# Kernel optimization log

Measured on AMD Instinct MI355X. Metric: run time of the kernel, lower is better.

The kernel has to match this reference:

```python
import jax, jax.numpy as jnp
import numpy as np

H = 12          # num_heads
LENS_T = 64     # template tokens
LENS_S = 256    # search tokens
KEEP = int(0.7 * LENS_S)  # 179 kept search tokens


def _ln(x, s, b):
    mu = jnp.mean(x, axis=-1, keepdims=True)
    var = jnp.mean(jnp.square(x - mu), axis=-1, keepdims=True)
    return (x - mu) / jnp.sqrt(var + 1e-5) * s + b


def setup_inputs() -> dict:
    key = jax.random.key(0)
    ks = jax.random.split(key, 8)
    B, C, Hh = 32, 768, 3072
    N = LENS_T + LENS_S
    w = lambda k, shape: jax.random.normal(k, shape, jnp.float32) * 0.02
    return {
        "x": jax.random.normal(ks[0], (B, N, C), jnp.float32),
        "global_index_t": jnp.tile(jnp.arange(LENS_T, dtype=jnp.int32), (B, 1)),
        "global_index_s": jnp.tile(jnp.arange(LENS_S, dtype=jnp.int32), (B, 1)),
        "norm1_s": jnp.ones((C,), jnp.float32), "norm1_b": jnp.zeros((C,), jnp.float32),
        "qkv_w": w(ks[1], (C, 3 * C)), "qkv_b": jnp.zeros((3 * C,), jnp.float32),
        "proj_w": w(ks[2], (C, C)), "proj_b": jnp.zeros((C,), jnp.float32),
        "norm2_s": jnp.ones((C,), jnp.float32), "norm2_b": jnp.zeros((C,), jnp.float32),
        "fc1_w": w(ks[3], (C, Hh)), "fc1_b": jnp.zeros((Hh,), jnp.float32),
        "fc2_w": w(ks[4], (Hh, C)), "fc2_b": jnp.zeros((C,), jnp.float32),
        "gcn_w": w(ks[5], (C, C)), "gcn_b": jnp.zeros((C,), jnp.float32),
        "norm3_s": jnp.ones((C,), jnp.float32), "norm3_b": jnp.zeros((C,), jnp.float32),
    }


def reference(x, global_index_t, global_index_s,
              norm1_s, norm1_b, qkv_w, qkv_b, proj_w, proj_b,
              norm2_s, norm2_b, fc1_w, fc1_b, fc2_w, fc2_b,
              gcn_w, gcn_b, norm3_s, norm3_b):
    B, N, C = x.shape
    hd = C // H
    scale = hd ** -0.5

    # --- attention (attn weights explicitly materialized) ---
    h = _ln(x, norm1_s, norm1_b)
    qkv = (h @ qkv_w + qkv_b).reshape(B, N, 3, H, hd).transpose(2, 0, 3, 1, 4)
    q, k, v = qkv[0], qkv[1], qkv[2]                      # [B,H,N,hd]
    attn = jax.nn.softmax(jnp.einsum('bhqd,bhkd->bhqk', q, k) * scale, axis=-1)
    xa = jnp.einsum('bhqk,bhkd->bhqd', attn, v).transpose(0, 2, 1, 3).reshape(B, N, C)
    xa = xa @ proj_w + proj_b
    x = x + xa

    # --- MLP ---
    x_res = x
    h2 = _ln(x, norm2_s, norm2_b)
    h2 = jax.nn.gelu(h2 @ fc1_w + fc1_b, approximate=False) @ fc2_w + fc2_b
    x = x_res + h2

    # --- GCN using template<->search attention as adjacency ---
    # adjacency = [[0, w_ts], [w_ts^T, 0]]; exploit block sparsity instead of
    # materializing the dense [B,N,N] matrix.
    w_ts = jnp.sum(attn[:, :, :LENS_T, LENS_T:], axis=1) / H   # [B,T,S]
    w_ts = jax.nn.softmax(w_ts, axis=2)
    support = x @ gcn_w + gcn_b
    out_t = jnp.einsum('bts,bsd->btd', w_ts, support[:, LENS_T:])   # top block
    out_s = jnp.einsum('bts,btd->bsd', w_ts, support[:, :LENS_T])   # bottom block
    x = jnp.concatenate([out_t, out_s], axis=1)
    x = x + _ln(x, norm3_s, norm3_b)

    # --- top-k token pruning on search tokens ---
    score_s = jnp.mean(attn[:, :, :LENS_T, LENS_T:], axis=(1, 2))   # [B,S]
    order = jnp.argsort(-score_s, axis=1)
    keep_indices = order[:, :KEEP]
    removed_index_s = order[:, KEEP:]
    gs_new = jnp.take_along_axis(global_index_s, keep_indices, axis=1)
    idx = jnp.concatenate([global_index_t.astype(jnp.int32), keep_indices + LENS_T], axis=1)
    x = jnp.take_along_axis(x, jnp.broadcast_to(idx[..., None], (B, idx.shape[1], C)), axis=1)
    return (x, global_index_t, gs_new, removed_index_s, attn)
```

## Files before the change

### kernel.cpp

```cpp
#include <hip/hip_runtime.h>
#include <math.h>

#define NKEEP 179
#define NREM  77
#define NOUT_ROWS 243

typedef __bf16 bf16x8 __attribute__((ext_vector_type(8)));
typedef float f32x4 __attribute__((ext_vector_type(4)));

__device__ __forceinline__ unsigned short f2bf(float f) {
  unsigned u = __builtin_bit_cast(unsigned, f);
  u = (u + 0x7FFFu + ((u >> 16) & 1u)) >> 16;
  return (unsigned short)u;
}

__device__ __forceinline__ void gload_lds16(const void* g, void* l) {
  __builtin_amdgcn_global_load_lds((const __attribute__((address_space(1))) void*)g,
                                   (__attribute__((address_space(3))) void*)l,
                                   16, 0, 0);
}

template<int RESID, int OUTMODE>
__global__ __launch_bounds__(256)
void ln_kernel(const float* __restrict__ in, const float* __restrict__ gs,
               const float* __restrict__ gb, void* __restrict__ outp,
               void* __restrict__ outp2) {
  int row = blockIdx.x;
  const float* p = in + (size_t)row * 768;
  int tid = threadIdx.x;
  float v0 = p[tid], v1 = p[tid + 256], v2 = p[tid + 512];
  __shared__ double rs[256], rq[256];
  double d0 = v0, d1 = v1, d2 = v2;
  rs[tid] = d0 + d1 + d2;
  rq[tid] = d0 * d0 + d1 * d1 + d2 * d2;
  __syncthreads();
  for (int st = 128; st > 0; st >>= 1) {
    if (tid < st) { rs[tid] += rs[tid + st]; rq[tid] += rq[tid + st]; }
    __syncthreads();
  }
  double mu  = rs[0] * (1.0 / 768.0);
  double var = rq[0] * (1.0 / 768.0) - mu * mu;
  float rstd = (float)rsqrt(var + 1e-5);
  float muf = (float)mu;
  float y0 = (v0 - muf) * rstd * gs[tid]       + gb[tid];
  float y1 = (v1 - muf) * rstd * gs[tid + 256] + gb[tid + 256];
  float y2 = (v2 - muf) * rstd * gs[tid + 512] + gb[tid + 512];
  if (RESID) { y0 += v0; y1 += v1; y2 += v2; }
  if (OUTMODE == 0 || OUTMODE == 2) {
    float* o = (float*)outp + (size_t)row * 768;
    o[tid] = y0; o[tid + 256] = y1; o[tid + 512] = y2;
  }
  if (OUTMODE == 1) {
    unsigned short* o = (unsigned short*)outp + (size_t)row * 768;
    o[tid] = f2bf(y0); o[tid + 256] = f2bf(y1); o[tid + 512] = f2bf(y2);
  }
  if (OUTMODE == 2) {
    unsigned short* o = (unsigned short*)outp2 + (size_t)row * 768;
    o[tid] = f2bf(y0); o[tid + 256] = f2bf(y1); o[tid + 512] = f2bf(y2);
  }
}

__global__ __launch_bounds__(256)
void wtrans_kernel(const float* __restrict__ W, unsigned short* __restrict__ Wt,
                   int K, int N) {
  __shared__ float t[32][33];
  int n0 = blockIdx.x * 32, k0 = blockIdx.y * 32;
  int tid = threadIdx.x;
#pragma unroll
  for (int p = 0; p < 4; p++) {
    int idx = tid + p * 256;
    int r = idx >> 5, c = idx & 31;
    t[r][c] = W[(size_t)(k0 + r) * N + n0 + c];
  }
  __syncthreads();
#pragma unroll
  for (int p = 0; p < 4; p++) {
    int idx = tid + p * 256;
    int r = idx >> 5, c = idx & 31;
    Wt[(size_t)(n0 + r) * K + k0 + c] = f2bf(t[c][r]);
  }
}

template<int ACT, int RES, int OUTBF>
__global__ __launch_bounds__(256)
void gemm_bf16_kernel(const unsigned short* __restrict__ A,
                      const unsigned short* __restrict__ Bt,
                      const float* __restrict__ bias, const float* __restrict__ res,
                      void* __restrict__ outp, int M, int K, int N) {
  __shared__ unsigned short Al[128 * 64];
  __shared__ unsigned short Bl[128 * 64];
  int tid = threadIdx.x;
  int lane = tid & 63, wid = tid >> 6;
  int wr = wid >> 1, wc = wid & 1;
  int bm0 = blockIdx.y * 128, bn0 = blockIdx.x * 128;

  int r8 = lane >> 3;
  int csw = lane & 7;
  int csrc = csw ^ r8;

  const unsigned short* Abase = A + (size_t)bm0 * K + (size_t)csrc * 8;
  const unsigned short* Bbase = Bt + (size_t)bn0 * K + (size_t)csrc * 8;

  f32x4 acc[4][4] = {};

  int mrow = lane & 15;
  int kch = lane >> 4;
  int key = mrow & 7;

  for (int k0 = 0; k0 < K; k0 += 64) {
#pragma unroll
    for (int i = 0; i < 4; i++) {
      int rr = wid * 32 + i * 8;
      gload_lds16(Abase + (size_t)(rr + r8) * K + k0, Al + rr * 64);
      gload_lds16(Bbase + (size_t)(rr + r8) * K + k0, Bl + rr * 64);
    }
    __syncthreads();
#pragma unroll
    for (int ks = 0; ks < 2; ks++) {
      bf16x8 af[4], bfr[4];
#pragma unroll
      for (int f = 0; f < 4; f++) {
        int ra = wr * 64 + f * 16 + mrow;
        int ca = (ks * 4 + kch) ^ key;
        af[f] = *reinterpret_cast<const bf16x8*>(&Al[ra * 64 + ca * 8]);
        int rb = wc * 64 + f * 16 + mrow;
        bfr[f] = *reinterpret_cast<const bf16x8*>(&Bl[rb * 64 + ca * 8]);
      }
#pragma unroll
      for (int fm = 0; fm < 4; fm++)
#pragma unroll
        for (int fn = 0; fn < 4; fn++)
          acc[fm][fn] = __builtin_amdgcn_mfma_f32_16x16x32_bf16(
              af[fm], bfr[fn], acc[fm][fn], 0, 0, 0);
    }
    __syncthreads();
  }
#pragma unroll
  for (int fm = 0; fm < 4; fm++) {
#pragma unroll
    for (int j = 0; j < 4; j++) {
      int row = bm0 + wr * 64 + fm * 16 + (lane >> 4) * 4 + j;
#pragma unroll
      for (int fn = 0; fn < 4; fn++) {
        int col = bn0 + wc * 64 + fn * 16 + (lane & 15);
        float c = acc[fm][fn][j] + bias[col];
        if (ACT == 1) c = 0.5f * c * (1.0f + erff(c * 0.70710678118654752f));
        if (RES) c += res[(size_t)row * N + col];
        if (OUTBF) ((unsigned short*)outp)[(size_t)row * N + col] = f2bf(c);
        else       ((float*)outp)[(size_t)row * N + col] = c;
      }
    }
  }
}

__global__ __launch_bounds__(256)
void gemm_qkv_bf16_kernel(const unsigned short* __restrict__ A,
                          const unsigned short* __restrict__ Bt,
                          const float* __restrict__ bias,
                          float* __restrict__ Qb, float* __restrict__ Kb,
                          float* __restrict__ Vb) {
  __shared__ unsigned short Al[128 * 64];
  __shared__ unsigned short Bl[128 * 64];
  const int K = 768;
  int tid = threadIdx.x;
  int lane = tid & 63, wid = tid >> 6;
  int wr = wid >> 1, wc = wid & 1;
  int bm0 = blockIdx.y * 128, bn0 = blockIdx.x * 128;

  int r8 = lane >> 3;
  int csw = lane & 7;
  int csrc = csw ^ r8;

  const unsigned short* Abase = A + (size_t)bm0 * K + (size_t)csrc * 8;
  const unsigned short* Bbase = Bt + (size_t)bn0 * K + (size_t)csrc * 8;

  f32x4 acc[4][4] = {};
  int mrow = lane & 15;
  int kch = lane >> 4;
  int key = mrow & 7;

  for (int k0 = 0; k0 < K; k0 += 64) {
#pragma unroll
    for (int i = 0; i < 4; i++) {
      int rr = wid * 32 + i * 8;
      gload_lds16(Abase + (size_t)(rr + r8) * K + k0, Al + rr * 64);
      gload_lds16(Bbase + (size_t)(rr + r8) * K + k0, Bl + rr * 64);
    }
    __syncthreads();
#pragma unroll
    for (int ks = 0; ks < 2; ks++) {
      bf16x8 af[4], bfr[4];
#pragma unroll
      for (int f = 0; f < 4; f++) {
        int ra = wr * 64 + f * 16 + mrow;
        int ca = (ks * 4 + kch) ^ key;
        af[f] = *reinterpret_cast<const bf16x8*>(&Al[ra * 64 + ca * 8]);
        int rb = wc * 64 + f * 16 + mrow;
        bfr[f] = *reinterpret_cast<const bf16x8*>(&Bl[rb * 64 + ca * 8]);
      }
#pragma unroll
      for (int fm = 0; fm < 4; fm++)
#pragma unroll
        for (int fn = 0; fn < 4; fn++)
          acc[fm][fn] = __builtin_amdgcn_mfma_f32_16x16x32_bf16(
              af[fm], bfr[fn], acc[fm][fn], 0, 0, 0);
    }
    __syncthreads();
  }
#pragma unroll
  for (int fm = 0; fm < 4; fm++) {
#pragma unroll
    for (int j = 0; j < 4; j++) {
      int row = bm0 + wr * 64 + fm * 16 + (lane >> 4) * 4 + j;
      int b = row / 320, nr = row - b * 320;
#pragma unroll
      for (int fn = 0; fn < 4; fn++) {
        int col = bn0 + wc * 64 + fn * 16 + (lane & 15);
        int sel = col / 768;
        int rem = col - sel * 768;
        int h = rem >> 6, d = rem & 63;
        float* dstb = (sel == 0) ? Qb : (sel == 1) ? Kb : Vb;
        dstb[(((size_t)(b * 12 + h) * 320 + nr) << 6) + d] = acc[fm][fn][j] + bias[col];
      }
    }
  }
}

template<int ROWMAP>
__global__ __launch_bounds__(256)
void gemm_prec_kernel(const float* __restrict__ A, const float* __restrict__ W,
                      const float* __restrict__ bias, int colOff,
                      float* __restrict__ Dst) {
  __shared__ float As[64][20];
  __shared__ float Bs[16][64];
  int tid = threadIdx.x;
  int tx = tid & 15, ty = tid >> 4;
  int bm0 = blockIdx.y * 64, bn0 = blockIdx.x * 64;
  int sm = tid >> 2, sc4 = tid & 3;
  int br = tid >> 4, bc4 = tid & 15;
  int arow;
  if (ROWMAP) { int m = bm0 + sm; arow = (m >> 6) * 320 + (m & 63); }
  else        { arow = bm0 + sm; }
  const float* Aptr = A + (size_t)arow * 768 + sc4 * 4;
  const float* Wptr = W + (size_t)br * 2304 + colOff + bn0 + bc4 * 4;

  double master[4][4] = {};
  for (int k0 = 0; k0 < 768; k0 += 16) {
    float4 av = *(const float4*)(Aptr + k0);
    float4 bv = *(const float4*)(Wptr + (size_t)k0 * 2304);
    __syncthreads();
    *(float4*)&As[sm][sc4 * 4] = av;
    *(float4*)&Bs[br][bc4 * 4] = bv;
    __syncthreads();
    float chunk[4][4] = {};
#pragma unroll
    for (int kk = 0; kk < 16; kk++) {
      float a[4], bb[4];
      *(float4*)bb = *(const float4*)&Bs[kk][tx * 4];
#pragma unroll
      for (int i = 0; i < 4; i++) a[i] = As[ty * 4 + i][kk];
#pragma unroll
      for (int i = 0; i < 4; i++)
#pragma unroll
        for (int j = 0; j < 4; j++) chunk[i][j] = fmaf(a[i], bb[j], chunk[i][j]);
    }
#pragma unroll
    for (int i = 0; i < 4; i++)
#pragma unroll
      for (int j = 0; j < 4; j++) master[i][j] += (double)chunk[i][j];
  }
  int n0 = bn0 + tx * 4;
  int h = n0 >> 6, d = n0 & 63;
#pragma unroll
  for (int i = 0; i < 4; i++) {
    int m = bm0 + ty * 4 + i;
    int b, nr;
    if (ROWMAP) { b = m >> 6; nr = m & 63; }
    else        { b = m / 320; nr = m - b * 320; }
    float* dst = Dst + (((size_t)(b * 12 + h) * 320 + nr) << 6) + d;
    float4 v;
    v.x = (float)master[i][0] + bias[colOff + n0];
    v.y = (float)master[i][1] + bias[colOff + n0 + 1];
    v.z = (float)master[i][2] + bias[colOff + n0 + 2];
    v.w = (float)master[i][3] + bias[colOff + n0 + 3];
    *(float4*)dst = v;
  }
}

__global__ __launch_bounds__(256)
void attn_fused_kernel(const float* __restrict__ Qb, const float* __restrict__ Kb,
                       const float* __restrict__ Vb, float* __restrict__ attn,
                       unsigned short* __restrict__ xa) {
  __shared__ float Qs[64][68];
  __shared__ float Ks[64][68];
  int qt = blockIdx.x, h = blockIdx.y, b = blockIdx.z;
  int bh = b * 12 + h;
  int q0 = qt * 64;
  int t = threadIdx.x;
  int tx = t & 15, ty = t >> 4;
  const float* Qg = Qb + (((size_t)bh * 320 + q0) << 6);
  const float* Kg = Kb + (((size_t)bh * 320) << 6);
  const float* Vg = Vb + (((size_t)bh * 320) << 6);
  float* attn_bh = attn + ((size_t)bh * 320 + q0) * 320;

  {
    int r = t >> 2, c = (t & 3) * 16;
    const float* src = Qg + (r << 6) + c;
#pragma unroll
    for (int i = 0; i < 4; i++)
      *(float4*)&Qs[r][c + i * 4] = *(const float4*)(src + i * 4);
  }

  float mrow[4] = {-1e30f, -1e30f, -1e30f, -1e30f};
  for (int kc = 0; kc < 5; ++kc) {
    __syncthreads();
    {
      int r = t >> 2, c = (t & 3) * 16;
      const float* src = Kg + ((size_t)(kc * 64 + r) << 6) + c;
#pragma unroll
      for (int i = 0; i < 4; i++)
        *(float4*)&Ks[r][c + i * 4] = *(const float4*)(src + i * 4);
    }
    __syncthreads();
    float acc[4][4] = {};
#pragma unroll 4
    for (int d0 = 0; d0 < 64; d0 += 4) {
      float4 qv[4], kv[4];
#pragma unroll
      for (int i = 0; i < 4; i++) qv[i] = *(const float4*)&Qs[ty * 4 + i][d0];
#pragma unroll
      for (int j = 0; j < 4; j++) kv[j] = *(const float4*)&Ks[tx * 4 + j][d0];
#pragma unroll
      for (int i = 0; i < 4; i++)
#pragma unroll
        for (int j = 0; j < 4; j++) {
          acc[i][j] = fmaf(qv[i].x, kv[j].x, acc[i][j]);
          acc[i][j] = fmaf(qv[i].y, kv[j].y, acc[i][j]);
          acc[i][j] = fmaf(qv[i].z, kv[j].z, acc[i][j]);
          acc[i][j] = fmaf(qv[i].w, kv[j].w, acc[i][j]);
        }
    }
#pragma unroll
    for (int i = 0; i < 4; i++) {
      float4 sv;
      sv.x = acc[i][0] * 0.125f; sv.y = acc[i][1] * 0.125f;
      sv.z = acc[i][2] * 0.125f; sv.w = acc[i][3] * 0.125f;
      mrow[i] = fmaxf(mrow[i], fmaxf(fmaxf(sv.x, sv.y), fmaxf(sv.z, sv.w)));
      *(float4*)&attn_bh[(size_t)(ty * 4 + i) * 320 + kc * 64 + tx * 4] = sv;
    }
  }
#pragma unroll
  for (int i = 0; i < 4; i++) {
    mrow[i] = fmaxf(mrow[i], __shfl_xor(mrow[i], 1, 16));
    mrow[i] = fmaxf(mrow[i], __shfl_xor(mrow[i], 2, 16));
    mrow[i] = fmaxf(mrow[i], __shfl_xor(mrow[i], 4, 16));
    mrow[i] = fmaxf(mrow[i], __shfl_xor(mrow[i], 8, 16));
  }
  __syncthreads();

  double lsum[4] = {0.0, 0.0, 0.0, 0.0};
#pragma unroll
  for (int i = 0; i < 4; i++) {
    float* rp = attn_bh + (size_t)(ty * 4 + i) * 320;
    for (int u = 0; u < 20; u++) {
      int k = tx + 16 * u;
      float e = expf(rp[k] - mrow[i]);
      rp[k] = e;
      lsum[i] += (double)e;
    }
  }
#pragma unroll
  for (int i = 0; i < 4; i++) {
    lsum[i] += __shfl_xor(lsum[i], 1, 16);
    lsum[i] += __shfl_xor(lsum[i], 2, 16);
    lsum[i] += __shfl_xor(lsum[i], 4, 16);
    lsum[i] += __shfl_xor(lsum[i], 8, 16);
  }
  float inv[4];
#pragma unroll
  for (int i = 0; i < 4; i++) inv[i] = (float)(1.0 / lsum[i]);
  __syncthreads();

#pragma unroll
  for (int i = 0; i < 4; i++) {
    float* rp = attn_bh + (size_t)(ty * 4 + i) * 320;
    for (int u = 0; u < 20; u++) {
      int k = tx + 16 * u;
      rp[k] *= inv[i];
    }
  }

  float acc2[4][4] = {};
  for (int kc = 0; kc < 5; ++kc) {
    __syncthreads();
    {
      int r = t >> 2, c = (t & 3) * 16;
      const float* src = Vg + ((size_t)(kc * 64 + r) << 6) + c;
#pragma unroll
      for (int i = 0; i < 4; i++)
        *(float4*)&Ks[r][c + i * 4] = *(const float4*)(src + i * 4);
    }
    __syncthreads();
#pragma unroll 4
    for (int kk4 = 0; kk4 < 16; ++kk4) {
      int k = kc * 64 + kk4 * 4;
      float4 pv[4], vv[4];
#pragma unroll
      for (int i = 0; i < 4; i++)
        pv[i] = *(const float4*)&attn_bh[(size_t)(ty * 4 + i) * 320 + k];
#pragma unroll
      for (int l = 0; l < 4; l++) vv[l] = *(const float4*)&Ks[kk4 * 4 + l][tx * 4];
#pragma unroll
      for (int i = 0; i < 4; i++) {
        acc2[i][0] = fmaf(pv[i].x, vv[0].x, acc2[i][0]);
        acc2[i][1] = fmaf(pv[i].x, vv[0].y, acc2[i][1]);
        acc2[i][2] = fmaf(pv[i].x, vv[0].z, acc2[i][2]);
        acc2[i][3] = fmaf(pv[i].x, vv[0].w, acc2[i][3]);
        acc2[i][0] = fmaf(pv[i].y, vv[1].x, acc2[i][0]);
        acc2[i][1] = fmaf(pv[i].y, vv[1].y, acc2[i][1]);
        acc2[i][2] = fmaf(pv[i].y, vv[1].z, acc2[i][2]);
        acc2[i][3] = fmaf(pv[i].y, vv[1].w, acc2[i][3]);
        acc2[i][0] = fmaf(pv[i].z, vv[2].x, acc2[i][0]);
        acc2[i][1] = fmaf(pv[i].z, vv[2].y, acc2[i][1]);
        acc2[i][2] = fmaf(pv[i].z, vv[2].z, acc2[i][2]);
        acc2[i][3] = fmaf(pv[i].z, vv[2].w, acc2[i][3]);
        acc2[i][0] = fmaf(pv[i].w, vv[3].x, acc2[i][0]);
        acc2[i][1] = fmaf(pv[i].w, vv[3].y, acc2[i][1]);
        acc2[i][2] = fmaf(pv[i].w, vv[3].z, acc2[i][2]);
        acc2[i][3] = fmaf(pv[i].w, vv[3].w, acc2[i][3]);
      }
    }
  }
#pragma unroll
  for (int i = 0; i < 4; i++) {
    unsigned short* dst = xa + (size_t)(b * 320 + q0 + ty * 4 + i) * 768 + h * 64 + tx * 4;
    uint2 pk;
    pk.x = (unsigned)f2bf(acc2[i][0]) | ((unsigned)f2bf(acc2[i][1]) << 16);
    pk.y = (unsigned)f2bf(acc2[i][2]) | ((unsigned)f2bf(acc2[i][3]) << 16);
    *(uint2*)dst = pk;
  }
}

__global__ __launch_bounds__(256)
void wts_kernel(const float* __restrict__ attn, float* __restrict__ wts) {
  int bid = blockIdx.x;
  int tt = bid & 63, b = bid >> 6;
  int s = threadIdx.x;
  float acc = 0.0f;
  const float* base = attn + (((size_t)(b * 12)) * 320 + tt) * 320 + 64 + s;
#pragma unroll
  for (int h = 0; h < 12; h++) acc += base[(size_t)h * 320 * 320];
  acc *= (1.0f / 12.0f);
  __shared__ float red[256];
  red[s] = acc; __syncthreads();
  for (int st = 128; st > 0; st >>= 1) {
    if (s < st) red[s] = fmaxf(red[s], red[s + st]);
    __syncthreads();
  }
  float m = red[0]; __syncthreads();
  float e = expf(acc - m);
  red[s] = e; __syncthreads();
  for (int st = 128; st > 0; st >>= 1) {
    if (s < st) red[s] += red[s + st];
    __syncthreads();
  }
  wts[(size_t)bid * 256 + s] = e / red[0];
}

__global__ __launch_bounds__(256)
void out_t_kernel(const float* __restrict__ wts, const float* __restrict__ sup,
                  float* __restrict__ x3) {
  int idx = blockIdx.x * 256 + threadIdx.x;
  int c = idx % 768;
  int tt = (idx / 768) % 64;
  int b = idx / (768 * 64);
  const float* wrow = wts + (size_t)(b * 64 + tt) * 256;
  const float* sp = sup + ((size_t)(b * 320 + 64)) * 768 + c;
  float acc = 0.0f;
  for (int s = 0; s < 256; s++) acc = fmaf(wrow[s], sp[(size_t)s * 768], acc);
  x3[((size_t)(b * 320 + tt)) * 768 + c] = acc;
}

__global__ __launch_bounds__(256)
void out_s_kernel(const float* __restrict__ wts, const float* __restrict__ sup,
                  float* __restrict__ x3) {
  int idx = blockIdx.x * 256 + threadIdx.x;
  int c = idx % 768;
  int s = (idx / 768) % 256;
  int b = idx / (768 * 256);
  const float* wp = wts + (size_t)(b * 64) * 256 + s;
  const float* sp = sup + ((size_t)(b * 320)) * 768 + c;
  float acc = 0.0f;
#pragma unroll 4
  for (int tt = 0; tt < 64; tt++) acc = fmaf(wp[(size_t)tt * 256], sp[(size_t)tt * 768], acc);
  x3[((size_t)(b * 320 + 64 + s)) * 768 + c] = acc;
}

__global__ __launch_bounds__(256)
void score_part_kernel(const float* __restrict__ attn, double* __restrict__ part) {
  int h = blockIdx.x, b = blockIdx.y;
  int s = threadIdx.x;
  const float* base = attn + (((size_t)(b * 12 + h)) * 320) * 320 + 64 + s;
  double acc = 0.0;
  for (int tt = 0; tt < 64; tt++) acc += (double)base[(size_t)tt * 320];
  part[((size_t)(b * 12 + h)) * 256 + s] = acc;
}

__global__ __launch_bounds__(256)
void score_final_kernel(const double* __restrict__ part, const int* __restrict__ git,
                        const int* __restrict__ gis, int* __restrict__ order_ws,
                        float* __restrict__ out_git, float* __restrict__ out_gs,
                        float* __restrict__ out_rm) {
  int b = blockIdx.x, s = threadIdx.x;
  double acc = 0.0;
#pragma unroll
  for (int h = 0; h < 12; h++) acc += part[((size_t)(b * 12 + h)) * 256 + s];
  __shared__ double sc[256];
  __shared__ int ord[256];
  sc[s] = acc;
  __syncthreads();
  double my = sc[s];
  int r = 0;
  for (int i = 0; i < 256; i++) {
    double si = sc[i];
    r += (si > my) || (si == my && i < s);
  }
  ord[r] = s;
  __syncthreads();
  int o = ord[s];
  order_ws[b * 256 + s] = o;
  if (s < NKEEP) out_gs[b * NKEEP + s] = (float)gis[b * 256 + o];
  else           out_rm[b * NREM + (s - NKEEP)] = (float)o;
  if (s < 64)    out_git[b * 64 + s] = (float)git[b * 64 + s];
}

__global__ __launch_bounds__(256)
void gather_kernel(const float* __restrict__ x3, const int* __restrict__ git,
                   const int* __restrict__ order_ws, float* __restrict__ out) {
  int bid = blockIdx.x;
  int j = bid % NOUT_ROWS, b = bid / NOUT_ROWS;
  int src = (j < 64) ? git[b * 64 + j] : (order_ws[b * 256 + (j - 64)] + 64);
  const float* p = x3 + ((size_t)(b * 320 + src)) * 768;
  float* o = out + ((size_t)(b * NOUT_ROWS + j)) * 768;
  int tid = threadIdx.x;
  o[tid] = p[tid]; o[tid + 256] = p[tid + 256]; o[tid + 512] = p[tid + 512];
}

extern "C" void kernel_launch(void* const* d_in, const int* in_sizes, int n_in,
                              void* d_out, int out_size, void* d_ws, size_t ws_size,
                              hipStream_t stream) {
  (void)in_sizes; (void)n_in; (void)out_size; (void)ws_size;
  const float* x      = (const float*)d_in[0];
  const int*   git    = (const int*)d_in[1];
  const int*   gis    = (const int*)d_in[2];
  const float* n1s    = (const float*)d_in[3];
  const float* n1b    = (const float*)d_in[4];
  const float* qkv_w  = (const float*)d_in[5];
  const float* qkv_b  = (const float*)d_in[6];
  const float* proj_w = (const float*)d_in[7];
  const float* proj_b = (const float*)d_in[8];
  const float* n2s    = (const float*)d_in[9];
  const float* n2b    = (const float*)d_in[10];
  const float* fc1_w  = (const float*)d_in[11];
  const float* fc1_b  = (const float*)d_in[12];
  const float* fc2_w  = (const float*)d_in[13];
  const float* fc2_b  = (const float*)d_in[14];
  const float* gcn_w  = (const float*)d_in[15];
  const float* gcn_b  = (const float*)d_in[16];
  const float* n3s    = (const float*)d_in[17];
  const float* n3b    = (const float*)d_in[18];

  float* out     = (float*)d_out;
  float* out_x   = out;
  float* out_git = out + 5971968;
  float* out_gs  = out + 5974016;
  float* out_rm  = out + 5979744;
  float* attn    = out + 5982208;

  float* w      = (float*)d_ws;
  float* bufA   = w;
  float* bufB   = w + 7864320;
  float* bufBIG = w + 15728640;
  float* Qbuf = bufBIG;
  float* Kbuf = bufBIG + 7864320;
  float* Vbuf = bufBIG + 15728640;
  unsigned short* ln1_bf = (unsigned short*)(bufBIG + 23592960);
  unsigned short* f1_bf = (unsigned short*)bufBIG;
  unsigned short* x2_bf = (unsigned short*)(bufBIG + 15728640);
  float* x3 = bufBIG + 19660800;
  unsigned short* wbf = (unsigned short*)(bufBIG + 27525120);
  unsigned short* proj_wt = wbf;
  unsigned short* fc1_wt  = wbf + 589824;
  unsigned short* fc2_wt  = fc1_wt + 2359296;
  unsigned short* gcn_wt  = fc2_wt + 2359296;
  unsigned short* qkv_wt  = gcn_wt + 589824;
  unsigned short* xa_bf = (unsigned short*)bufA;
  unsigned short* h2_bf = (unsigned short*)bufA;
  float* wts    = bufBIG + 31457280;
  int*   order_ws = (int*)(wts + 524288);
  double* partd  = (double*)(wts + 524288 + 8192);

  const int M = 10240;

  wtrans_kernel<<<dim3(24, 24), dim3(256), 0, stream>>>(proj_w, proj_wt, 768, 768);
  wtrans_kernel<<<dim3(96, 24), dim3(256), 0, stream>>>(fc1_w, fc1_wt, 768, 3072);
  wtrans_kernel<<<dim3(24, 96), dim3(256), 0, stream>>>(fc2_w, fc2_wt, 3072, 768);
  wtrans_kernel<<<dim3(24, 24), dim3(256), 0, stream>>>(gcn_w, gcn_wt, 768, 768);
  wtrans_kernel<<<dim3(72, 24), dim3(256), 0, stream>>>(qkv_w, qkv_wt, 768, 2304);

  ln_kernel<0, 2><<<dim3(M), dim3(256), 0, stream>>>(x, n1s, n1b, bufA, ln1_bf);
  gemm_qkv_bf16_kernel<<<dim3(18, 80), dim3(256), 0, stream>>>(
      ln1_bf, qkv_wt, qkv_b, Qbuf, Kbuf, Vbuf);
  gemm_prec_kernel<0><<<dim3(12, 160), dim3(256), 0, stream>>>(
      bufA, qkv_w, qkv_b, 768, Kbuf);
  gemm_prec_kernel<1><<<dim3(12, 32), dim3(256), 0, stream>>>(
      bufA, qkv_w, qkv_b, 0, Qbuf);
  attn_fused_kernel<<<dim3(5, 12, 32), dim3(256), 0, stream>>>(
      Qbuf, Kbuf, Vbuf, attn, xa_bf);
  gemm_bf16_kernel<0, 1, 0><<<dim3(768 / 128, M / 128), dim3(256), 0, stream>>>(
      xa_bf, proj_wt, proj_b, x, bufB, M, 768, 768);
  ln_kernel<0, 1><<<dim3(M), dim3(256), 0, stream>>>(bufB, n2s, n2b, h2_bf, nullptr);
  gemm_bf16_kernel<1, 0, 1><<<dim3(3072 / 128, M / 128), dim3(256), 0, stream>>>(
      h2_bf, fc1_wt, fc1_b, nullptr, f1_bf, M, 768, 3072);
  gemm_bf16_kernel<0, 1, 1><<<dim3(768 / 128, M / 128), dim3(256), 0, stream>>>(
      f1_bf, fc2_wt, fc2_b, bufB, x2_bf, M, 3072, 768);
  wts_kernel<<<dim3(32 * 64), dim3(256), 0, stream>>>(attn, wts);
  gemm_bf16_kernel<0, 0, 0><<<dim3(768 / 128, M / 128), dim3(256), 0, stream>>>(
      x2_bf, gcn_wt, gcn_b, nullptr, bufA, M, 768, 768);
  out_t_kernel<<<dim3(32 * 64 * 768 / 256), dim3(256), 0, stream>>>(wts, bufA, x3);
  out_s_kernel<<<dim3(32 * 256 * 768 / 256), dim3(256), 0, stream>>>(wts, bufA, x3);
  ln_kernel<1, 0><<<dim3(M), dim3(256), 0, stream>>>(x3, n3s, n3b, x3, nullptr);
  score_part_kernel<<<dim3(12, 32), dim3(256), 0, stream>>>(attn, partd);
  score_final_kernel<<<dim3(32), dim3(256), 0, stream>>>(partd, git, gis, order_ws,
                                                         out_git, out_gs, out_rm);
  gather_kernel<<<dim3(32 * NOUT_ROWS), dim3(256), 0, stream>>>(x3, git,
                                                                order_ws, out_x);
}
```

Baseline: 1.093 ms.

## Enlarge precise GEMM tile and keep attention scores in registers for softmax

The fp32/fp64-accumulating precise GEMM used for K and Q now computes 128x64 tiles with a 32-deep K step instead of 64x64 with 16. This doubles per-thread work, halves the grid and cuts barrier count. The attention kernel keeps the 4x20 score values per thread in registers through max, exp and normalisation and writes the attn matrix to global memory once. Previously it wrote, reread, rewrote, reread and rewrote it. The cost is higher register pressure from the larger double accumulator array and the score array, which may lower occupancy.

```diff
diff --git a/kernel.cpp b/kernel.cpp
--- a/kernel.cpp
+++ b/kernel.cpp
@@ -231,59 +231,91 @@
 void gemm_prec_kernel(const float* __restrict__ A, const float* __restrict__ W,
                       const float* __restrict__ bias, int colOff,
                       float* __restrict__ Dst) {
-  __shared__ float As[64][20];
-  __shared__ float Bs[16][64];
+  __shared__ float As[128][36];
+  __shared__ float Bs[32][68];
   int tid = threadIdx.x;
   int tx = tid & 15, ty = tid >> 4;
-  int bm0 = blockIdx.y * 64, bn0 = blockIdx.x * 64;
-  int sm = tid >> 2, sc4 = tid & 3;
-  int br = tid >> 4, bc4 = tid & 15;
-  int arow;
-  if (ROWMAP) { int m = bm0 + sm; arow = (m >> 6) * 320 + (m & 63); }
-  else        { arow = bm0 + sm; }
-  const float* Aptr = A + (size_t)arow * 768 + sc4 * 4;
-  const float* Wptr = W + (size_t)br * 2304 + colOff + bn0 + bc4 * 4;
-
-  double master[4][4] = {};
-  for (int k0 = 0; k0 < 768; k0 += 16) {
-    float4 av = *(const float4*)(Aptr + k0);
-    float4 bv = *(const float4*)(Wptr + (size_t)k0 * 2304);
-    __syncthreads();
-    *(float4*)&As[sm][sc4 * 4] = av;
-    *(float4*)&Bs[br][bc4 * 4] = bv;
-    __syncthreads();
-    float chunk[4][4] = {};
-#pragma unroll
-    for (int kk = 0; kk < 16; kk++) {
-      float a[4], bb[4];
-      *(float4*)bb = *(const float4*)&Bs[kk][tx * 4];
-#pragma unroll
-      for (int i = 0; i < 4; i++) a[i] = As[ty * 4 + i][kk];
-#pragma unroll
-      for (int i = 0; i < 4; i++)
-#pragma unroll
-        for (int j = 0; j < 4; j++) chunk[i][j] = fmaf(a[i], bb[j], chunk[i][j]);
-    }
-#pragma unroll
-    for (int i = 0; i < 4; i++)
-#pragma unroll
-      for (int j = 0; j < 4; j++) master[i][j] += (double)chunk[i][j];
+  int bm0 = blockIdx.y * 128, bn0 = blockIdx.x * 64;
+
+  int ar[4];
+#pragma unroll
+  for (int q = 0; q < 4; q++) {
+    int idx = tid + q * 256;
+    int r = idx >> 3;
+    int m = bm0 + r;
+    ar[q] = ROWMAP ? ((m >> 6) * 320 + (m & 63)) : m;
+  }
+  const float* Wbase = W + colOff + bn0;
+
+  double master[8][4] = {};
+  for (int k0 = 0; k0 < 768; k0 += 32) {
+    float4 av[4], bv[2];
+#pragma unroll
+    for (int q = 0; q < 4; q++) {
+      int idx = tid + q * 256;
+      av[q] = *(const float4*)(A + (size_t)ar[q] * 768 + k0 + (idx & 7) * 4);
+    }
+#pragma unroll
+    for (int q = 0; q < 2; q++) {
+      int idx = tid + q * 256;
+      int br = idx >> 4, bc4 = idx & 15;
+      bv[q] = *(const float4*)(Wbase + (size_t)(k0 + br) * 2304 + bc4 * 4);
+    }
+    __syncthreads();
+#pragma unroll
+    for (int q = 0; q < 4; q++) {
+      int idx = tid + q * 256;
+      *(float4*)&As[idx >> 3][(idx & 7) * 4] = av[q];
+    }
+#pragma unroll
+    for (int q = 0; q < 2; q++) {
+      int idx = tid + q * 256;
+      *(float4*)&Bs[idx >> 4][(idx & 15) * 4] = bv[q];
+    }
+    __syncthreads();
+#pragma unroll
+    for (int half = 0; half < 2; half++) {
+      float chunk[8][4] = {};
+#pragma unroll
+      for (int kk = 0; kk < 16; kk++) {
+        int kkk = half * 16 + kk;
+        float a[8], bb[4];
+        *(float4*)bb = *(const float4*)&Bs[kkk][tx * 4];
+#pragma unroll
+        for (int i = 0; i < 4; i++) {
+          a[i]     = As[ty * 4 + i][kkk];
+          a[4 + i] = As[64 + ty * 4 + i][kkk];
+        }
+#pragma unroll
+        for (int i = 0; i < 8; i++)
+#pragma unroll
+          for (int j = 0; j < 4; j++) chunk[i][j] = fmaf(a[i], bb[j], chunk[i][j]);
+      }
+#pragma unroll
+      for (int i = 0; i < 8; i++)
+#pragma unroll
+        for (int j = 0; j < 4; j++) master[i][j] += (double)chunk[i][j];
+    }
+    __syncthreads();
   }
   int n0 = bn0 + tx * 4;
   int h = n0 >> 6, d = n0 & 63;
 #pragma unroll
-  for (int i = 0; i < 4; i++) {
-    int m = bm0 + ty * 4 + i;
-    int b, nr;
-    if (ROWMAP) { b = m >> 6; nr = m & 63; }
-    else        { b = m / 320; nr = m - b * 320; }
-    float* dst = Dst + (((size_t)(b * 12 + h) * 320 + nr) << 6) + d;
-    float4 v;
-    v.x = (float)master[i][0] + bias[colOff + n0];
-    v.y = (float)master[i][1] + bias[colOff + n0 + 1];
-    v.z = (float)master[i][2] + bias[colOff + n0 + 2];
-    v.w = (float)master[i][3] + bias[colOff + n0 + 3];
-    *(float4*)dst = v;
+  for (int g = 0; g < 2; g++) {
+#pragma unroll
+    for (int i = 0; i < 4; i++) {
+      int m = bm0 + g * 64 + ty * 4 + i;
+      int b, nr;
+      if (ROWMAP) { b = m >> 6; nr = m & 63; }
+      else        { b = m / 320; nr = m - b * 320; }
+      float* dst = Dst + (((size_t)(b * 12 + h) * 320 + nr) << 6) + d;
+      float4 v;
+      v.x = (float)master[g * 4 + i][0] + bias[colOff + n0];
+      v.y = (float)master[g * 4 + i][1] + bias[colOff + n0 + 1];
+      v.z = (float)master[g * 4 + i][2] + bias[colOff + n0 + 2];
+      v.w = (float)master[g * 4 + i][3] + bias[colOff + n0 + 3];
+      *(float4*)dst = v;
+    }
   }
 }
 
@@ -311,7 +343,10 @@
       *(float4*)&Qs[r][c + i * 4] = *(const float4*)(src + i * 4);
   }
 
+  float s[4][20];
   float mrow[4] = {-1e30f, -1e30f, -1e30f, -1e30f};
+
+#pragma unroll
   for (int kc = 0; kc < 5; ++kc) {
     __syncthreads();
     {
@@ -342,11 +377,11 @@
     }
 #pragma unroll
     for (int i = 0; i < 4; i++) {
-      float4 sv;
-      sv.x = acc[i][0] * 0.125f; sv.y = acc[i][1] * 0.125f;
-      sv.z = acc[i][2] * 0.125f; sv.w = acc[i][3] * 0.125f;
-      mrow[i] = fmaxf(mrow[i], fmaxf(fmaxf(sv.x, sv.y), fmaxf(sv.z, sv.w)));
-      *(float4*)&attn_bh[(size_t)(ty * 4 + i) * 320 + kc * 64 + tx * 4] = sv;
+      float sx = acc[i][0] * 0.125f, sy = acc[i][1] * 0.125f;
+      float sz = acc[i][2] * 0.125f, sw = acc[i][3] * 0.125f;
+      mrow[i] = fmaxf(mrow[i], fmaxf(fmaxf(sx, sy), fmaxf(sz, sw)));
+      s[i][kc * 4 + 0] = sx; s[i][kc * 4 + 1] = sy;
+      s[i][kc * 4 + 2] = sz; s[i][kc * 4 + 3] = sw;
     }
   }
 #pragma unroll
@@ -356,19 +391,16 @@
     mrow[i] = fmaxf(mrow[i], __shfl_xor(mrow[i], 4, 16));
     mrow[i] = fmaxf(mrow[i], __shfl_xor(mrow[i], 8, 16));
   }
-  __syncthreads();
 
   double lsum[4] = {0.0, 0.0, 0.0, 0.0};
 #pragma unroll
-  for (int i = 0; i < 4; i++) {
-    float* rp = attn_bh + (size_t)(ty * 4 + i) * 320;
-    for (int u = 0; u < 20; u++) {
-      int k = tx + 16 * u;
-      float e = expf(rp[k] - mrow[i]);
-      rp[k] = e;
+  for (int i = 0; i < 4; i++)
+#pragma unroll
+    for (int c = 0; c < 20; c++) {
+      float e = expf(s[i][c] - mrow[i]);
+      s[i][c] = e;
       lsum[i] += (double)e;
     }
-  }
 #pragma unroll
   for (int i = 0; i < 4; i++) {
     lsum[i] += __shfl_xor(lsum[i], 1, 16);
@@ -379,16 +411,19 @@
   float inv[4];
 #pragma unroll
   for (int i = 0; i < 4; i++) inv[i] = (float)(1.0 / lsum[i]);
+
+#pragma unroll
+  for (int i = 0; i < 4; i++)
+#pragma unroll
+    for (int kc = 0; kc < 5; kc++) {
+      float4 sv;
+      sv.x = s[i][kc * 4 + 0] * inv[i];
+      sv.y = s[i][kc * 4 + 1] * inv[i];
+      sv.z = s[i][kc * 4 + 2] * inv[i];
+      sv.w = s[i][kc * 4 + 3] * inv[i];
+      *(float4*)&attn_bh[(size_t)(ty * 4 + i) * 320 + kc * 64 + tx * 4] = sv;
+    }
   __syncthreads();
-
-#pragma unroll
-  for (int i = 0; i < 4; i++) {
-    float* rp = attn_bh + (size_t)(ty * 4 + i) * 320;
-    for (int u = 0; u < 20; u++) {
-      int k = tx + 16 * u;
-      rp[k] *= inv[i];
-    }
-  }
 
   float acc2[4][4] = {};
   for (int kc = 0; kc < 5; ++kc) {
@@ -611,9 +646,9 @@
   ln_kernel<0, 2><<<dim3(M), dim3(256), 0, stream>>>(x, n1s, n1b, bufA, ln1_bf);
   gemm_qkv_bf16_kernel<<<dim3(18, 80), dim3(256), 0, stream>>>(
       ln1_bf, qkv_wt, qkv_b, Qbuf, Kbuf, Vbuf);
-  gemm_prec_kernel<0><<<dim3(12, 160), dim3(256), 0, stream>>>(
+  gemm_prec_kernel<0><<<dim3(12, 80), dim3(256), 0, stream>>>(
       bufA, qkv_w, qkv_b, 768, Kbuf);
-  gemm_prec_kernel<1><<<dim3(12, 32), dim3(256), 0, stream>>>(
+  gemm_prec_kernel<1><<<dim3(12, 16), dim3(256), 0, stream>>>(
       bufA, qkv_w, qkv_b, 0, Qbuf);
   attn_fused_kernel<<<dim3(5, 12, 32), dim3(256), 0, stream>>>(
       Qbuf, Kbuf, Vbuf, attn, xa_bf);
```

Result: slower. 1.304 ms (+19.3%).

## Skip redundant K columns in bf16 QKV GEMM and keep softmax scores in registers

Applied to the files above, without the earlier changes.

The bf16 QKV GEMM no longer computes the K third of the output, which was overwritten anyway by the higher-precision K GEMM. This cuts its grid from 18 to 12 column tiles. The attention kernel now holds the scaled scores for each thread in registers (4x20 floats) and writes the normalized attention to global memory once. Previously it did three read-modify-write passes over the attn buffer. This raises register pressure in the attention kernel, which may lower occupancy.

```diff
diff --git a/kernel.cpp b/kernel.cpp
--- a/kernel.cpp
+++ b/kernel.cpp
@@ -157,22 +157,23 @@
 void gemm_qkv_bf16_kernel(const unsigned short* __restrict__ A,
                           const unsigned short* __restrict__ Bt,
                           const float* __restrict__ bias,
-                          float* __restrict__ Qb, float* __restrict__ Kb,
-                          float* __restrict__ Vb) {
+                          float* __restrict__ Qb, float* __restrict__ Vb) {
   __shared__ unsigned short Al[128 * 64];
   __shared__ unsigned short Bl[128 * 64];
   const int K = 768;
   int tid = threadIdx.x;
   int lane = tid & 63, wid = tid >> 6;
   int wr = wid >> 1, wc = wid & 1;
-  int bm0 = blockIdx.y * 128, bn0 = blockIdx.x * 128;
+  int bx = blockIdx.x;
+  int colbase = (bx < 6) ? bx * 128 : (bx - 6) * 128 + 1536;
+  int bm0 = blockIdx.y * 128;
 
   int r8 = lane >> 3;
   int csw = lane & 7;
   int csrc = csw ^ r8;
 
   const unsigned short* Abase = A + (size_t)bm0 * K + (size_t)csrc * 8;
-  const unsigned short* Bbase = Bt + (size_t)bn0 * K + (size_t)csrc * 8;
+  const unsigned short* Bbase = Bt + (size_t)colbase * K + (size_t)csrc * 8;
 
   f32x4 acc[4][4] = {};
   int mrow = lane & 15;
@@ -215,11 +216,11 @@
       int b = row / 320, nr = row - b * 320;
 #pragma unroll
       for (int fn = 0; fn < 4; fn++) {
-        int col = bn0 + wc * 64 + fn * 16 + (lane & 15);
+        int col = colbase + wc * 64 + fn * 16 + (lane & 15);
         int sel = col / 768;
         int rem = col - sel * 768;
         int h = rem >> 6, d = rem & 63;
-        float* dstb = (sel == 0) ? Qb : (sel == 1) ? Kb : Vb;
+        float* dstb = (sel == 0) ? Qb : Vb;
         dstb[(((size_t)(b * 12 + h) * 320 + nr) << 6) + d] = acc[fm][fn][j] + bias[col];
       }
     }
@@ -311,7 +312,10 @@
       *(float4*)&Qs[r][c + i * 4] = *(const float4*)(src + i * 4);
   }
 
+  float s[4][20];
   float mrow[4] = {-1e30f, -1e30f, -1e30f, -1e30f};
+
+#pragma unroll
   for (int kc = 0; kc < 5; ++kc) {
     __syncthreads();
     {
@@ -342,11 +346,11 @@
     }
 #pragma unroll
     for (int i = 0; i < 4; i++) {
-      float4 sv;
-      sv.x = acc[i][0] * 0.125f; sv.y = acc[i][1] * 0.125f;
-      sv.z = acc[i][2] * 0.125f; sv.w = acc[i][3] * 0.125f;
-      mrow[i] = fmaxf(mrow[i], fmaxf(fmaxf(sv.x, sv.y), fmaxf(sv.z, sv.w)));
-      *(float4*)&attn_bh[(size_t)(ty * 4 + i) * 320 + kc * 64 + tx * 4] = sv;
+      float sx = acc[i][0] * 0.125f, sy = acc[i][1] * 0.125f;
+      float sz = acc[i][2] * 0.125f, sw = acc[i][3] * 0.125f;
+      mrow[i] = fmaxf(mrow[i], fmaxf(fmaxf(sx, sy), fmaxf(sz, sw)));
+      s[i][kc * 4 + 0] = sx; s[i][kc * 4 + 1] = sy;
+      s[i][kc * 4 + 2] = sz; s[i][kc * 4 + 3] = sw;
     }
   }
 #pragma unroll
@@ -356,19 +360,16 @@
     mrow[i] = fmaxf(mrow[i], __shfl_xor(mrow[i], 4, 16));
     mrow[i] = fmaxf(mrow[i], __shfl_xor(mrow[i], 8, 16));
   }
-  __syncthreads();
 
   double lsum[4] = {0.0, 0.0, 0.0, 0.0};
 #pragma unroll
-  for (int i = 0; i < 4; i++) {
-    float* rp = attn_bh + (size_t)(ty * 4 + i) * 320;
-    for (int u = 0; u < 20; u++) {
-      int k = tx + 16 * u;
-      float e = expf(rp[k] - mrow[i]);
-      rp[k] = e;
+  for (int i = 0; i < 4; i++)
+#pragma unroll
+    for (int c = 0; c < 20; c++) {
+      float e = expf(s[i][c] - mrow[i]);
+      s[i][c] = e;
       lsum[i] += (double)e;
     }
-  }
 #pragma unroll
   for (int i = 0; i < 4; i++) {
     lsum[i] += __shfl_xor(lsum[i], 1, 16);
@@ -379,16 +380,19 @@
   float inv[4];
 #pragma unroll
   for (int i = 0; i < 4; i++) inv[i] = (float)(1.0 / lsum[i]);
+
+#pragma unroll
+  for (int i = 0; i < 4; i++)
+#pragma unroll
+    for (int kc = 0; kc < 5; kc++) {
+      float4 sv;
+      sv.x = s[i][kc * 4 + 0] * inv[i];
+      sv.y = s[i][kc * 4 + 1] * inv[i];
+      sv.z = s[i][kc * 4 + 2] * inv[i];
+      sv.w = s[i][kc * 4 + 3] * inv[i];
+      *(float4*)&attn_bh[(size_t)(ty * 4 + i) * 320 + kc * 64 + tx * 4] = sv;
+    }
   __syncthreads();
-
-#pragma unroll
-  for (int i = 0; i < 4; i++) {
-    float* rp = attn_bh + (size_t)(ty * 4 + i) * 320;
-    for (int u = 0; u < 20; u++) {
-      int k = tx + 16 * u;
-      rp[k] *= inv[i];
-    }
-  }
 
   float acc2[4][4] = {};
   for (int kc = 0; kc < 5; ++kc) {
@@ -609,8 +613,8 @@
   wtrans_kernel<<<dim3(72, 24), dim3(256), 0, stream>>>(qkv_w, qkv_wt, 768, 2304);
 
   ln_kernel<0, 2><<<dim3(M), dim3(256), 0, stream>>>(x, n1s, n1b, bufA, ln1_bf);
-  gemm_qkv_bf16_kernel<<<dim3(18, 80), dim3(256), 0, stream>>>(
-      ln1_bf, qkv_wt, qkv_b, Qbuf, Kbuf, Vbuf);
+  gemm_qkv_bf16_kernel<<<dim3(12, 80), dim3(256), 0, stream>>>(
+      ln1_bf, qkv_wt, qkv_b, Qbuf, Vbuf);
   gemm_prec_kernel<0><<<dim3(12, 160), dim3(256), 0, stream>>>(
       bufA, qkv_w, qkv_b, 768, Kbuf);
   gemm_prec_kernel<1><<<dim3(12, 32), dim3(256), 0, stream>>>(
```

After: 1.058 ms. -3.2%, faster.
